# Kernel optimization log

Measured on AMD Instinct MI355X. Metric: run time of the kernel, lower is better.

Reference implementation:

```python
import jax, jax.numpy as jnp
import numpy as np

T, D = 1024, 2048
H, KH, HD = 16, 4, 128
E, K, I = 8, 2, 2048
EPS = 1e-5
CAP = 30.0          # attn logit softcap and router logit softcap
BASE = 10000.0      # rope theta


def setup_inputs() -> dict:
    key = jax.random.key(0)
    ks = jax.random.split(key, 8)
    s = 0.02
    return {
        "positions": jnp.arange(T, dtype=jnp.int32),
        "hidden_states": jax.random.normal(ks[0], (T, D), jnp.float32),
        "w_qkv": jax.random.normal(ks[1], (D, (H + 2 * KH) * HD), jnp.float32) * s,
        "w_o": jax.random.normal(ks[2], (H * HD, D), jnp.float32) * s,
        "w_gate": jax.random.normal(ks[3], (D, E), jnp.float32) * s,
        "w_gate_up": jax.random.normal(ks[4], (E, D, 2 * I), jnp.float32) * s,
        "w_down": jax.random.normal(ks[5], (E, I, D), jnp.float32) * s,
        "w_pre_attn": 1.0 + 0.01 * jax.random.normal(ks[6], (D,), jnp.float32),
        "w_post_attn": jnp.ones((D,), jnp.float32),
        "w_pre_moe": 1.0 + 0.01 * jax.random.normal(ks[7], (D,), jnp.float32),
        "w_post_moe": jnp.ones((D,), jnp.float32),
    }


def rmsnorm(x, w):
    v = jnp.mean(jnp.square(x), axis=-1, keepdims=True)
    return x * jax.lax.rsqrt(v + EPS) * w


def rope_neox(pos, x):
    # x: [T, nH, HD]; full-head-dim neox-style rotation
    half = HD // 2
    inv = 1.0 / (BASE ** (jnp.arange(half, dtype=jnp.float32) * 2.0 / HD))
    f = pos.astype(jnp.float32)[:, None] * inv            # [T, half]
    cos, sin = jnp.cos(f)[:, None, :], jnp.sin(f)[:, None, :]
    x1, x2 = x[..., :half], x[..., half:]
    return jnp.concatenate([x1 * cos - x2 * sin, x2 * cos + x1 * sin], axis=-1)


def attention(pos, x, w_qkv, w_o):
    qkv = x @ w_qkv
    q, k, v = jnp.split(qkv, [H * HD, (H + KH) * HD], axis=-1)
    q = rope_neox(pos, q.reshape(T, H, HD))
    k = rope_neox(pos, k.reshape(T, KH, HD))
    v = v.reshape(T, KH, HD)
    rep = H // KH                                          # GQA repeat
    k = jnp.repeat(k, rep, axis=1)
    v = jnp.repeat(v, rep, axis=1)
    s = jnp.einsum('qhd,khd->hqk', q, k) * (HD ** -0.5)
    s = CAP * jnp.tanh(s / CAP)                            # tanh logit cap
    causal = pos[:, None] >= pos[None, :]
    s = jnp.where(causal[None], s, -1e30)
    p = jax.nn.softmax(s, axis=-1)
    o = jnp.einsum('hqk,khd->qhd', p, v).reshape(T, H * HD)
    return o @ w_o


def moe(x, w_gate, w_gate_up, w_down):
    logits = x @ w_gate
    logits = CAP * jnp.tanh(logits / CAP)                  # router softcap
    probs = jax.nn.softmax(logits, axis=-1)
    topv, topi = jax.lax.top_k(probs, K)                   # no renorm (Grok1)
    comb = jnp.zeros((T, E), probs.dtype).at[jnp.arange(T)[:, None], topi].set(topv)
    gu = jnp.einsum('td,edf->etf', x, w_gate_up)           # [E,T,2I]
    g, u = jnp.split(gu, 2, axis=-1)
    act = jax.nn.gelu(g, approximate=True) * u             # GeluAndMul(tanh)
    out_e = jnp.einsum('eti,eid->etd', act, w_down)        # [E,T,D]
    return jnp.einsum('etd,te->td', out_e, comb)


def reference(positions, hidden_states, w_qkv, w_o, w_gate, w_gate_up, w_down,
              w_pre_attn, w_post_attn, w_pre_moe, w_post_moe):
    resid = hidden_states
    h = rmsnorm(hidden_states, w_pre_attn)
    a = attention(positions, h, w_qkv, w_o)
    resid = resid + rmsnorm(a, w_post_attn)                # post_attn_norm + add
    h = rmsnorm(resid, w_pre_moe)
    m = moe(h, w_gate, w_gate_up, w_down)
    return resid + rmsnorm(m, w_post_moe)
```

## Files before the change

### kernel.cpp

```cpp
#include <hip/hip_runtime.h>

#define TT 1024
#define DD 2048
#define NH 16
#define NKV 4
#define HDIM 128
#define NE 8
#define NI 2048
#define EPSF 1e-5f
#define NP 4

typedef short bf16x8 __attribute__((ext_vector_type(8)));
typedef float f32x4 __attribute__((ext_vector_type(4)));

__device__ __forceinline__ unsigned short f2bf(float x) {
  unsigned u = __float_as_uint(x);
  u += 0x7FFFu + ((u >> 16) & 1u);
  return (unsigned short)(u >> 16);
}
__device__ __forceinline__ float bf2f(unsigned short h) {
  return __uint_as_float((unsigned)h << 16);
}
__device__ __forceinline__ void split2(float a, unsigned short& h,
                                       unsigned short& l) {
  h = f2bf(a);
  l = f2bf(a - bf2f(h));
}

__device__ __forceinline__ float wave_sum(float v) {
#pragma unroll
  for (int m = 32; m >= 1; m >>= 1) v += __shfl_xor(v, m, 64);
  return v;
}
__device__ __forceinline__ float wave_max(float v) {
#pragma unroll
  for (int m = 32; m >= 1; m >>= 1) v = fmaxf(v, __shfl_xor(v, m, 64));
  return v;
}

__device__ __forceinline__ int swz4(int r) { return (r ^ (r >> 2)) & 3; }
__device__ __forceinline__ int swz8(int r) { return (r ^ (r >> 3)) & 7; }

__device__ __forceinline__ void stage32(char* dst, const unsigned short* src,
                                        int rs, int tid) {
#pragma unroll
  for (int j = 0; j < 2; ++j) {
    int idx = tid + j * 256;
    int r = idx >> 2, c = idx & 3;
    bf16x8 v = *(const bf16x8*)(src + r * rs + c * 8);
    *(bf16x8*)(dst + r * 64 + ((c ^ swz4(r)) << 4)) = v;
  }
}
__device__ __forceinline__ void ld_frag(const char* base, int wrow, int l15,
                                        int lg, bf16x8* dst) {
#pragma unroll
  for (int i = 0; i < 4; ++i) {
    int row = wrow + i * 16 + l15;
    dst[i] = *(const bf16x8*)(base + row * 64 + ((lg ^ swz4(row)) << 4));
  }
}
__device__ __forceinline__ void mm16(const bf16x8* xa, const bf16x8* xb,
                                     f32x4 (*acc)[4]) {
#pragma unroll
  for (int mi = 0; mi < 4; ++mi)
#pragma unroll
    for (int ni = 0; ni < 4; ++ni)
      acc[mi][ni] = __builtin_amdgcn_mfma_f32_16x16x32_bf16(
          xa[mi], xb[ni], acc[mi][ni], 0, 0, 0);
}

template <int MODE>
__global__ __launch_bounds__(256) void pgemm3_k(
    const unsigned short* __restrict__ Ah, const unsigned short* __restrict__ Al,
    const unsigned short* __restrict__ Bh, const unsigned short* __restrict__ Bl,
    float* __restrict__ C, int Kh, int lda, int ldb, int ldc, long czs,
    float escale) {
  int z = blockIdx.z;
  int m0 = blockIdx.y * 128, n0 = blockIdx.x * 128;
  int k0 = 0, kend = Kh;
  if (MODE == 0) {
    k0 = z * Kh;
    kend = k0 + Kh;
    C += (long)z * czs;
  } else if (MODE == 1) {
    if (blockIdx.x > blockIdx.y) return;
    Ah += (long)z * TT * lda;
    Al += (long)z * TT * lda;
    Bh += (long)(z >> 2) * TT * ldb;
    Bl += (long)(z >> 2) * TT * ldb;
    C += (long)z * czs;
  } else {
    int head = z >> 2, ch = z & 3;
    int limit = (blockIdx.y + 1) * 128;
    k0 = ch * 256;
    if (k0 >= limit) return;
    kend = k0 + 256 < limit ? k0 + 256 : limit;
    Ah += (long)head * TT * lda;
    Al += (long)head * TT * lda;
    Bh += (long)(head >> 2) * HDIM * ldb;
    Bl += (long)(head >> 2) * HDIM * ldb;
    C += (long)ch * czs + head * HDIM;
  }

  __shared__ __align__(16) char lds[32768];
  int tid = threadIdx.x, lane = tid & 63, wid = tid >> 6;
  int wm = (wid >> 1) * 64, wn = (wid & 1) * 64;
  int l15 = lane & 15, lg = lane >> 4;

  f32x4 acc[4][4];
#pragma unroll
  for (int i = 0; i < 4; ++i)
#pragma unroll
    for (int j = 0; j < 4; ++j) acc[i][j] = {0.f, 0.f, 0.f, 0.f};

  for (int kt = k0; kt < kend; kt += 32) {
    __syncthreads();
    stage32(lds, Ah + (long)m0 * lda + kt, lda, tid);
    stage32(lds + 8192, Al + (long)m0 * lda + kt, lda, tid);
    stage32(lds + 16384, Bh + (long)n0 * ldb + kt, ldb, tid);
    stage32(lds + 24576, Bl + (long)n0 * ldb + kt, ldb, tid);
    __syncthreads();
    bf16x8 fah[4], fal[4], fbh[4], fbl[4];
    ld_frag(lds, wm, l15, lg, fah);
    ld_frag(lds + 16384, wn, l15, lg, fbh);
    mm16(fah, fbh, acc);
    ld_frag(lds + 24576, wn, l15, lg, fbl);
    mm16(fah, fbl, acc);
    ld_frag(lds + 8192, wm, l15, lg, fal);
    mm16(fal, fbh, acc);
  }
#pragma unroll
  for (int mi = 0; mi < 4; ++mi)
#pragma unroll
    for (int ni = 0; ni < 4; ++ni)
#pragma unroll
      for (int rr = 0; rr < 4; ++rr) {
        int ml = m0 + wm + mi * 16 + lg * 4 + rr;
        int col = n0 + wn + ni * 16 + l15;
        float val = acc[mi][ni][rr];
        if (MODE == 1) {
          val *= escale;
          val = 30.f * tanhf(val * (1.f / 30.f));
        }
        C[(long)ml * ldc + col] = val;
      }
}

template <int AMODE, int EP>
__global__ __launch_bounds__(256) void gemm_k(
    const unsigned short* __restrict__ A, const float* __restrict__ Bf,
    float* __restrict__ Cf, int N, int K, int lda, int ldb, int ldc, long bzs,
    long pzs, const int* __restrict__ cnt, const int* __restrict__ basep,
    const int* __restrict__ tok, const int* __restrict__ slotp,
    const float* __restrict__ wtp, float* __restrict__ slots_out) {
  int z = blockIdx.z;
  int e = z >> 1, kp = z & 1;
  Bf += (long)e * bzs;
  int Me = cnt[e], be = basep[e];
  int m0 = blockIdx.y * 128, n0 = blockIdx.x * 128;
  if (m0 >= Me) return;
  int Kc = K >> 1, kbeg = kp * Kc, klim = kbeg + Kc;

  __shared__ __align__(16) char lds[32768];
  const int BOFF = 16384;
  int tid = threadIdx.x, lane = tid & 63, wid = tid >> 6;
  int wm = (wid >> 1) * 64, wn = (wid & 1) * 64;
  int l15 = lane & 15, lg = lane >> 4;

  f32x4 acc[4][4];
#pragma unroll
  for (int i = 0; i < 4; ++i)
#pragma unroll
    for (int j = 0; j < 4; ++j) acc[i][j] = {0.f, 0.f, 0.f, 0.f};

  for (int kt = kbeg; kt < klim; kt += 64) {
    __syncthreads();
#pragma unroll
    for (int i = 0; i < 4; ++i) {
      int idx = tid + i * 256;
      int r = idx >> 3, c = idx & 7;
      int gm = m0 + r;
      bf16x8 v = {0, 0, 0, 0, 0, 0, 0, 0};
      bool ok = gm < Me;
      long arow;
      if (AMODE == 1)
        arow = ok ? (long)tok[e * TT + gm] : 0;
      else
        arow = (long)be + gm;
      if (ok) v = *(const bf16x8*)(A + arow * (long)lda + kt + c * 8);
      *(bf16x8*)(lds + r * 128 + ((c ^ swz8(r)) << 4)) = v;
    }
#pragma unroll
    for (int i = 0; i < 4; ++i) {
      int gidx = tid + i * 256;
      int n = gidx & 127, kc = gidx >> 7;
      const float* src = Bf + (long)(kt + kc * 8) * ldb + n0 + n;
      bf16x8 v;
#pragma unroll
      for (int u = 0; u < 8; ++u)
        ((unsigned short*)&v)[u] = f2bf(src[(long)u * ldb]);
      *(bf16x8*)(lds + BOFF + n * 128 + ((kc ^ swz8(n)) << 4)) = v;
    }
    __syncthreads();
#pragma unroll
    for (int s = 0; s < 2; ++s) {
      bf16x8 af[4], bfr[4];
      int slotk = s * 4 + lg;
#pragma unroll
      for (int mi = 0; mi < 4; ++mi) {
        int row = wm + mi * 16 + l15;
        af[mi] =
            *(const bf16x8*)(lds + row * 128 + ((slotk ^ swz8(row)) << 4));
      }
#pragma unroll
      for (int ni = 0; ni < 4; ++ni) {
        int row = wn + ni * 16 + l15;
        bfr[ni] = *(const bf16x8*)(lds + BOFF + row * 128 +
                                   ((slotk ^ swz8(row)) << 4));
      }
      mm16(af, bfr, acc);
    }
  }
#pragma unroll
  for (int mi = 0; mi < 4; ++mi)
#pragma unroll
    for (int ni = 0; ni < 4; ++ni)
#pragma unroll
      for (int rr = 0; rr < 4; ++rr) {
        int ml = m0 + wm + mi * 16 + lg * 4 + rr;
        int col = n0 + wn + ni * 16 + l15;
        float val = acc[mi][ni][rr];
        if (ml < Me) {
          if (EP == 0) {
            Cf[(long)kp * pzs + (long)(be + ml) * ldc + col] = val;
          } else {
            int t = tok[e * TT + ml];
            int s = slotp[e * TT + ml];
            float w = wtp[e * TT + ml];
            slots_out[(long)kp * pzs + ((long)s * TT + t) * DD + col] =
                val * w;
          }
        }
      }
}

__global__ __launch_bounds__(256) void tsplit_k(const float* __restrict__ W,
                                                unsigned short* __restrict__ Th,
                                                unsigned short* __restrict__ Tl,
                                                int K, int N) {
  __shared__ float lds[64 * 65];
  int n0 = blockIdx.x * 64, k0 = blockIdx.y * 64;
  int tid = threadIdx.x;
#pragma unroll
  for (int i = 0; i < 4; ++i) {
    int idx = tid + i * 256;
    int kr = idx >> 4, cg = idx & 15;
    float4 v = *(const float4*)(W + (long)(k0 + kr) * N + n0 + cg * 4);
    float* p = &lds[kr * 65 + cg * 4];
    p[0] = v.x; p[1] = v.y; p[2] = v.z; p[3] = v.w;
  }
  __syncthreads();
#pragma unroll
  for (int i = 0; i < 2; ++i) {
    int idx = tid + i * 256;
    int n = idx >> 3, kc = idx & 7;
    bf16x8 h8, l8;
#pragma unroll
    for (int u = 0; u < 8; ++u) {
      unsigned short hh, ll;
      split2(lds[(kc * 8 + u) * 65 + n], hh, ll);
      ((unsigned short*)&h8)[u] = hh;
      ((unsigned short*)&l8)[u] = ll;
    }
    long o = (long)(n0 + n) * K + k0 + kc * 8;
    *(bf16x8*)(Th + o) = h8;
    *(bf16x8*)(Tl + o) = l8;
  }
}

__global__ __launch_bounds__(256) void rms_pre_k(const float* __restrict__ x,
                                                 const float* __restrict__ w,
                                                 unsigned short* __restrict__ oh,
                                                 unsigned short* __restrict__ ol) {
  __shared__ float red[4];
  int t = blockIdx.x, tid = threadIdx.x;
  const float* xr = x + (long)t * DD;
  float xv[8];
  float ss = 0.f;
#pragma unroll
  for (int i = 0; i < 8; ++i) {
    float v = xr[tid + i * 256];
    xv[i] = v;
    ss += v * v;
  }
  ss = wave_sum(ss);
  if ((tid & 63) == 0) red[tid >> 6] = ss;
  __syncthreads();
  float r = rsqrtf((red[0] + red[1] + red[2] + red[3]) * (1.f / DD) + EPSF);
#pragma unroll
  for (int i = 0; i < 8; ++i) {
    int d = tid + i * 256;
    split2(xv[i] * r * w[d], oh[(long)t * DD + d], ol[(long)t * DD + d]);
  }
}

__global__ __launch_bounds__(256) void rope_qk_k(
    const int* __restrict__ pos, const float* __restrict__ qp,
    unsigned short* __restrict__ qh, unsigned short* __restrict__ ql,
    unsigned short* __restrict__ kh, unsigned short* __restrict__ kl) {
  __shared__ float cs[64], sn[64];
  int t = blockIdx.x, tid = threadIdx.x;
  float pf = (float)pos[t];
  if (tid < 64) {
    float inv = exp2f(-(float)tid * 0.20762050593046015f);
    float f = pf * inv;
    cs[tid] = cosf(f);
    sn[tid] = sinf(f);
  }
  __syncthreads();
  const float* row = qp + (long)t * 3072;
  const long PS = (long)TT * 3072;
#pragma unroll
  for (int i = 0; i < 4; ++i) {
    int idx = tid + i * 256;
    int h = idx >> 6, j = idx & 63;
    float x1 = 0.f, x2 = 0.f;
#pragma unroll
    for (int p = 0; p < NP; ++p) {
      x1 += row[p * PS + h * HDIM + j];
      x2 += row[p * PS + h * HDIM + 64 + j];
    }
    float c = cs[j], s = sn[j];
    long base = ((long)h * TT + t) * HDIM;
    split2(x1 * c - x2 * s, qh[base + j], ql[base + j]);
    split2(x2 * c + x1 * s, qh[base + 64 + j], ql[base + 64 + j]);
  }
  {
    int k2 = tid >> 6, j = tid & 63;
    float x1 = 0.f, x2 = 0.f;
#pragma unroll
    for (int p = 0; p < NP; ++p) {
      x1 += row[p * PS + 2048 + k2 * HDIM + j];
      x2 += row[p * PS + 2048 + k2 * HDIM + 64 + j];
    }
    float c = cs[j], s = sn[j];
    long base = ((long)k2 * TT + t) * HDIM;
    split2(x1 * c - x2 * s, kh[base + j], kl[base + j]);
    split2(x2 * c + x1 * s, kh[base + 64 + j], kl[base + 64 + j]);
  }
}

__global__ __launch_bounds__(256) void vtrans_k(const float* __restrict__ qp,
                                                unsigned short* __restrict__ Vh,
                                                unsigned short* __restrict__ Vl) {
  __shared__ float lds[64 * 129];
  int tb = blockIdx.x, kv = blockIdx.y;
  int t0 = tb * 128;
  int tid = threadIdx.x;
  const long PS = (long)TT * 3072;
#pragma unroll
  for (int dh = 0; dh < 2; ++dh) {
    if (dh) __syncthreads();
#pragma unroll
    for (int i = 0; i < 8; ++i) {
      int fidx = tid + i * 256;
      int t = fidx >> 4, dq = fidx & 15;
      long gi = (long)(t0 + t) * 3072 + 2560 + kv * HDIM + dh * 64 + dq * 4;
      float4 a = *(const float4*)(qp + gi);
#pragma unroll
      for (int p = 1; p < NP; ++p) {
        float4 b = *(const float4*)(qp + p * PS + gi);
        a.x += b.x; a.y += b.y; a.z += b.z; a.w += b.w;
      }
      lds[(dq * 4 + 0) * 129 + t] = a.x;
      lds[(dq * 4 + 1) * 129 + t] = a.y;
      lds[(dq * 4 + 2) * 129 + t] = a.z;
      lds[(dq * 4 + 3) * 129 + t] = a.w;
    }
    __syncthreads();
#pragma unroll
    for (int i = 0; i < 4; ++i) {
      int cidx = tid + i * 256;
      int d = cidx >> 4, tc = cidx & 15;
      bf16x8 h8, l8;
#pragma unroll
      for (int u = 0; u < 8; ++u) {
        unsigned short hh, ll;
        split2(lds[d * 129 + tc * 8 + u], hh, ll);
        ((unsigned short*)&h8)[u] = hh;
        ((unsigned short*)&l8)[u] = ll;
      }
      long o = ((long)kv * HDIM + dh * 64 + d) * TT + t0 + tc * 8;
      *(bf16x8*)(Vh + o) = h8;
      *(bf16x8*)(Vl + o) = l8;
    }
  }
}

__global__ __launch_bounds__(256) void softmax_k(const float* __restrict__ S,
                                                 unsigned short* __restrict__ Ph,
                                                 unsigned short* __restrict__ Pl) {
  __shared__ float red[4];
  int i = blockIdx.x, h = blockIdx.y, tid = threadIdx.x;
  int len = i + 1;
  int wlimit = ((i >> 7) + 1) << 7;
  const float* srow = S + ((long)h * TT + i) * TT;
  unsigned short* ph = Ph + ((long)h * TT + i) * TT;
  unsigned short* pl = Pl + ((long)h * TT + i) * TT;
  float m = -1e30f;
  for (int j = tid; j < len; j += 256) m = fmaxf(m, srow[j]);
  m = wave_max(m);
  if ((tid & 63) == 0) red[tid >> 6] = m;
  __syncthreads();
  m = fmaxf(fmaxf(red[0], red[1]), fmaxf(red[2], red[3]));
  __syncthreads();
  float ssum = 0.f;
  for (int j = tid; j < len; j += 256) ssum += expf(srow[j] - m);
  ssum = wave_sum(ssum);
  if ((tid & 63) == 0) red[tid >> 6] = ssum;
  __syncthreads();
  float inv = 1.f / (red[0] + red[1] + red[2] + red[3]);
  for (int j = tid; j < wlimit; j += 256) {
    float p = (j < len) ? expf(srow[j] - m) * inv : 0.f;
    unsigned short hh, ll;
    split2(p, hh, ll);
    ph[j] = hh;
    pl[j] = ll;
  }
}

__global__ __launch_bounds__(256) void obreduce_k(const float* __restrict__ obp,
                                                  unsigned short* __restrict__ oh,
                                                  unsigned short* __restrict__ ol) {
  int m = blockIdx.x, tid = threadIdx.x;
  int nv = ((m >> 7) >> 1) + 1;
#pragma unroll
  for (int i = 0; i < 8; ++i) {
    int d = tid + i * 256;
    float s = 0.f;
    for (int c = 0; c < nv; ++c) s += obp[(long)c * TT * DD + (long)m * DD + d];
    split2(s, oh[(long)m * DD + d], ol[(long)m * DD + d]);
  }
}

__global__ __launch_bounds__(256) void post_attn_k(
    const float* __restrict__ ap, const float* __restrict__ hidden,
    const float* __restrict__ w_post, const float* __restrict__ w_pre2,
    float* __restrict__ resid1, float* __restrict__ h2f,
    unsigned short* __restrict__ h2b) {
  __shared__ float red[4];
  int t = blockIdx.x, tid = threadIdx.x;
  const long PS = (long)TT * DD;
  float av[8];
  float ss = 0.f;
#pragma unroll
  for (int i = 0; i < 8; ++i) {
    long o = (long)t * DD + tid + i * 256;
    float v = 0.f;
#pragma unroll
    for (int p = 0; p < NP; ++p) v += ap[p * PS + o];
    av[i] = v;
    ss += v * v;
  }
  ss = wave_sum(ss);
  if ((tid & 63) == 0) red[tid >> 6] = ss;
  __syncthreads();
  float r1 = rsqrtf((red[0] + red[1] + red[2] + red[3]) * (1.f / DD) + EPSF);
  __syncthreads();
  float rv[8];
  float ss2 = 0.f;
#pragma unroll
  for (int i = 0; i < 8; ++i) {
    int d = tid + i * 256;
    float v = hidden[(long)t * DD + d] + av[i] * r1 * w_post[d];
    rv[i] = v;
    resid1[(long)t * DD + d] = v;
    ss2 += v * v;
  }
  ss2 = wave_sum(ss2);
  if ((tid & 63) == 0) red[tid >> 6] = ss2;
  __syncthreads();
  float r2 = rsqrtf((red[0] + red[1] + red[2] + red[3]) * (1.f / DD) + EPSF);
#pragma unroll
  for (int i = 0; i < 8; ++i) {
    int d = tid + i * 256;
    float hv = rv[i] * r2 * w_pre2[d];
    h2f[(long)t * DD + d] = hv;
    h2b[(long)t * DD + d] = f2bf(hv);
  }
}

__global__ __launch_bounds__(256) void gate_k(const float* __restrict__ h2f,
                                              const float* __restrict__ wg,
                                              int* cnt, int* tok, int* slotp,
                                              float* wtp) {
  __shared__ float red[4][8];
  int t = blockIdx.x, tid = threadIdx.x;
  float a[8] = {0, 0, 0, 0, 0, 0, 0, 0};
  const float* x = h2f + (long)t * DD;
  for (int d = tid; d < DD; d += 256) {
    float xv = x[d];
    const float* wr = wg + d * 8;
#pragma unroll
    for (int e = 0; e < 8; ++e) a[e] += xv * wr[e];
  }
#pragma unroll
  for (int e = 0; e < 8; ++e) a[e] = wave_sum(a[e]);
  if ((tid & 63) == 0) {
#pragma unroll
    for (int e = 0; e < 8; ++e) red[tid >> 6][e] = a[e];
  }
  __syncthreads();
  if (tid == 0) {
    float l[8], p[8];
    float m = -1e30f;
    for (int e = 0; e < 8; ++e) {
      float v = red[0][e] + red[1][e] + red[2][e] + red[3][e];
      v = 30.f * tanhf(v * (1.f / 30.f));
      l[e] = v;
      m = fmaxf(m, v);
    }
    float s = 0.f;
    for (int e = 0; e < 8; ++e) { p[e] = expf(l[e] - m); s += p[e]; }
    for (int e = 0; e < 8; ++e) p[e] /= s;
    int i1 = 0;
    for (int e = 1; e < 8; ++e) if (p[e] > p[i1]) i1 = e;
    int i2 = (i1 == 0) ? 1 : 0;
    for (int e = 0; e < 8; ++e) if (e != i1 && p[e] > p[i2]) i2 = e;
    int q1 = atomicAdd(&cnt[i1], 1);
    tok[i1 * TT + q1] = t; slotp[i1 * TT + q1] = 0; wtp[i1 * TT + q1] = p[i1];
    int q2 = atomicAdd(&cnt[i2], 1);
    tok[i2 * TT + q2] = t; slotp[i2 * TT + q2] = 1; wtp[i2 * TT + q2] = p[i2];
  }
}

__global__ void scan_k(const int* __restrict__ cnt, int* __restrict__ basep) {
  if (threadIdx.x == 0) {
    int s = 0;
    for (int e = 0; e < NE; ++e) { basep[e] = s; s += cnt[e]; }
    basep[NE] = s;
  }
}

__global__ __launch_bounds__(256) void act_k(const float* __restrict__ gu,
                                             unsigned short* __restrict__ actb) {
  long a = blockIdx.x;
  const long PS = (long)2 * TT * 2 * NI;
  const float* g0 = gu + a * (2 * NI);
  const float* g1 = g0 + PS;
  for (int i = threadIdx.x; i < NI; i += 256) {
    float gg = g0[i] + g1[i];
    float uu = g0[i + NI] + g1[i + NI];
    float c = gg + 0.044715f * gg * gg * gg;
    float act = 0.5f * gg * (1.f + tanhf(0.7978845608028654f * c));
    actb[a * NI + i] = f2bf(act * uu);
  }
}

__global__ __launch_bounds__(256) void final_k(const float* __restrict__ resid1,
                                               const float* __restrict__ slots,
                                               const float* __restrict__ w2,
                                               float* __restrict__ out) {
  __shared__ float red[4];
  int t = blockIdx.x, tid = threadIdx.x;
  const long PL = (long)TT * DD;
  float mv[8];
  float ss = 0.f;
#pragma unroll
  for (int i = 0; i < 8; ++i) {
    long o = (long)t * DD + tid + i * 256;
    float v = slots[o] + slots[PL + o] + slots[2 * PL + o] + slots[3 * PL + o];
    mv[i] = v;
    ss += v * v;
  }
  ss = wave_sum(ss);
  if ((tid & 63) == 0) red[tid >> 6] = ss;
  __syncthreads();
  float r = rsqrtf((red[0] + red[1] + red[2] + red[3]) * (1.f / DD) + EPSF);
#pragma unroll
  for (int i = 0; i < 8; ++i) {
    int d = tid + i * 256;
    out[(long)t * DD + d] = resid1[(long)t * DD + d] + mv[i] * r * w2[d];
  }
}

__global__ void sentinel_k(float* out) { out[threadIdx.x] = 12345.0f; }

extern "C" void kernel_launch(void* const* d_in, const int* in_sizes, int n_in,
                              void* d_out, int out_size, void* d_ws,
                              size_t ws_size, hipStream_t stream) {
  const int* pos = (const int*)d_in[0];
  const float* hidden = (const float*)d_in[1];
  const float* w_qkv = (const float*)d_in[2];
  const float* w_o = (const float*)d_in[3];
  const float* w_gate = (const float*)d_in[4];
  const float* w_gu = (const float*)d_in[5];
  const float* w_down = (const float*)d_in[6];
  const float* w_pre_attn = (const float*)d_in[7];
  const float* w_post_attn = (const float*)d_in[8];
  const float* w_pre_moe = (const float*)d_in[9];
  const float* w_post_moe = (const float*)d_in[10];
  float* out = (float*)d_out;

  char* ws = (char*)d_ws;
  size_t off = 0;
  auto alloc = [&](size_t bytes) {
    char* p = ws + off;
    off += (bytes + 255) & ~(size_t)255;
    return p;
  };
  typedef unsigned short u16;
  u16* h1h = (u16*)alloc((size_t)TT * DD * 2);
  u16* h1l = (u16*)alloc((size_t)TT * DD * 2);
  u16* wqkvTh = (u16*)alloc((size_t)3072 * DD * 2);
  u16* wqkvTl = (u16*)alloc((size_t)3072 * DD * 2);
  float* qkvp = (float*)alloc((size_t)NP * TT * 3072 * 4);
  u16* qh_ = (u16*)alloc((size_t)NH * TT * HDIM * 2);
  u16* ql_ = (u16*)alloc((size_t)NH * TT * HDIM * 2);
  u16* kh_ = (u16*)alloc((size_t)NKV * TT * HDIM * 2);
  u16* kl_ = (u16*)alloc((size_t)NKV * TT * HDIM * 2);
  u16* vth = (u16*)alloc((size_t)NKV * HDIM * TT * 2);
  u16* vtl = (u16*)alloc((size_t)NKV * HDIM * TT * 2);
  float* S = (float*)alloc((size_t)NH * TT * TT * 4);
  u16* Ph = (u16*)alloc((size_t)NH * TT * TT * 2);
  u16* Pl = (u16*)alloc((size_t)NH * TT * TT * 2);
  float* obp = (float*)alloc((size_t)4 * TT * DD * 4);
  u16* obh = (u16*)alloc((size_t)TT * DD * 2);
  u16* obl = (u16*)alloc((size_t)TT * DD * 2);
  u16* woTh = (u16*)alloc((size_t)DD * DD * 2);
  u16* woTl = (u16*)alloc((size_t)DD * DD * 2);
  float* attnp = (float*)alloc((size_t)NP * TT * DD * 4);
  float* resid1 = (float*)alloc((size_t)TT * DD * 4);
  float* h2f = (float*)alloc((size_t)TT * DD * 4);
  u16* h2b = (u16*)alloc((size_t)TT * DD * 2);
  int* cnt = (int*)alloc(NE * 4);
  int* basep = (int*)alloc((NE + 1) * 4);
  int* tok = (int*)alloc((size_t)NE * TT * 4);
  int* slotp = (int*)alloc((size_t)NE * TT * 4);
  float* wtp = (float*)alloc((size_t)NE * TT * 4);
  float* gu = (float*)alloc((size_t)2 * 2 * TT * 2 * NI * 4);
  u16* actb = (u16*)alloc((size_t)2 * TT * NI * 2);
  float* slots = (float*)alloc((size_t)2 * 2 * TT * DD * 4);

  if (off > ws_size) {
    sentinel_k<<<1, 256, 0, stream>>>(out);
    return;
  }

  hipMemsetAsync(cnt, 0, NE * 4, stream);
  dim3 blk(256);

  rms_pre_k<<<TT, blk, 0, stream>>>(hidden, w_pre_attn, h1h, h1l);
  tsplit_k<<<dim3(3072 / 64, DD / 64), blk, 0, stream>>>(w_qkv, wqkvTh, wqkvTl,
                                                         DD, 3072);
  tsplit_k<<<dim3(DD / 64, DD / 64), blk, 0, stream>>>(w_o, woTh, woTl, DD, DD);

  pgemm3_k<0><<<dim3(3072 / 128, TT / 128, NP), blk, 0, stream>>>(
      h1h, h1l, wqkvTh, wqkvTl, qkvp, DD / NP, DD, DD, 3072, (long)TT * 3072,
      0.f);

  rope_qk_k<<<TT, blk, 0, stream>>>(pos, qkvp, qh_, ql_, kh_, kl_);
  vtrans_k<<<dim3(8, NKV), blk, 0, stream>>>(qkvp, vth, vtl);

  pgemm3_k<1><<<dim3(TT / 128, TT / 128, NH), blk, 0, stream>>>(
      qh_, ql_, kh_, kl_, S, HDIM, HDIM, HDIM, TT, (long)TT * TT,
      0.08838834764831845f);

  softmax_k<<<dim3(TT, NH), blk, 0, stream>>>(S, Ph, Pl);

  pgemm3_k<2><<<dim3(1, TT / 128, NH * 4), blk, 0, stream>>>(
      Ph, Pl, vth, vtl, obp, 256, TT, TT, DD, (long)TT * DD, 0.f);
  obreduce_k<<<TT, blk, 0, stream>>>(obp, obh, obl);

  pgemm3_k<0><<<dim3(DD / 128, TT / 128, NP), blk, 0, stream>>>(
      obh, obl, woTh, woTl, attnp, DD / NP, DD, DD, DD, (long)TT * DD, 0.f);

  post_attn_k<<<TT, blk, 0, stream>>>(attnp, hidden, w_post_attn, w_pre_moe,
                                      resid1, h2f, h2b);
  gate_k<<<TT, blk, 0, stream>>>(h2f, w_gate, cnt, tok, slotp, wtp);
  scan_k<<<1, 64, 0, stream>>>(cnt, basep);

  gemm_k<1, 0><<<dim3(2 * NI / 128, TT / 128, NE * 2), blk, 0, stream>>>(
      h2b, w_gu, gu, 2 * NI, DD, DD, 2 * NI, 2 * NI, (long)DD * 2 * NI,
      (long)2 * TT * 2 * NI, cnt, basep, tok, nullptr, nullptr, nullptr);

  act_k<<<2 * TT, blk, 0, stream>>>(gu, actb);

  gemm_k<2, 3><<<dim3(DD / 128, TT / 128, NE * 2), blk, 0, stream>>>(
      actb, w_down, nullptr, DD, NI, NI, DD, DD, (long)NI * DD,
      (long)2 * TT * DD, cnt, basep, tok, slotp, wtp, slots);

  final_k<<<TT, blk, 0, stream>>>(resid1, slots, w_post_moe, out);
}
```

Measured before the change: 491.2 us.

## Process two M-blocks per MoE GEMM block and store intermediates as bf16

The MoE expert GEMM now handles up to 256 token rows per block in two 128-row sub-tiles. Each fp32-to-bf16 converted weight tile is loaded once and reused across both sub-tiles, which halves the redundant weight reads and conversions. The gate/up partials and down-projection slot outputs are also written as bf16 instead of fp32, reducing intermediate memory traffic for act_k and final_k. The cost is doubled accumulator registers and more LDS, which may lower occupancy, plus some extra rounding in the partial sums.

```diff
diff --git a/kernel.cpp b/kernel.cpp
--- a/kernel.cpp
+++ b/kernel.cpp
@@ -149,47 +149,36 @@
 template <int AMODE, int EP>
 __global__ __launch_bounds__(256) void gemm_k(
     const unsigned short* __restrict__ A, const float* __restrict__ Bf,
-    float* __restrict__ Cf, int N, int K, int lda, int ldb, int ldc, long bzs,
-    long pzs, const int* __restrict__ cnt, const int* __restrict__ basep,
-    const int* __restrict__ tok, const int* __restrict__ slotp,
-    const float* __restrict__ wtp, float* __restrict__ slots_out) {
+    unsigned short* __restrict__ Cb, int N, int K, int lda, int ldb, int ldc,
+    long bzs, long pzs, const int* __restrict__ cnt,
+    const int* __restrict__ basep, const int* __restrict__ tok,
+    const int* __restrict__ slotp, const float* __restrict__ wtp,
+    unsigned short* __restrict__ slots_out) {
   int z = blockIdx.z;
   int e = z >> 1, kp = z & 1;
   Bf += (long)e * bzs;
   int Me = cnt[e], be = basep[e];
-  int m0 = blockIdx.y * 128, n0 = blockIdx.x * 128;
-  if (m0 >= Me) return;
+  int ms0 = blockIdx.y * 256, n0 = blockIdx.x * 128;
+  if (ms0 >= Me) return;
+  int nmb = (Me - ms0 > 128) ? 2 : 1;
   int Kc = K >> 1, kbeg = kp * Kc, klim = kbeg + Kc;
 
-  __shared__ __align__(16) char lds[32768];
-  const int BOFF = 16384;
+  __shared__ __align__(16) char lds[49152];
+  const int BOFF = 32768;
   int tid = threadIdx.x, lane = tid & 63, wid = tid >> 6;
   int wm = (wid >> 1) * 64, wn = (wid & 1) * 64;
   int l15 = lane & 15, lg = lane >> 4;
 
-  f32x4 acc[4][4];
-#pragma unroll
-  for (int i = 0; i < 4; ++i)
-#pragma unroll
-    for (int j = 0; j < 4; ++j) acc[i][j] = {0.f, 0.f, 0.f, 0.f};
+  f32x4 acc[2][4][4];
+#pragma unroll
+  for (int b = 0; b < 2; ++b)
+#pragma unroll
+    for (int i = 0; i < 4; ++i)
+#pragma unroll
+      for (int j = 0; j < 4; ++j) acc[b][i][j] = {0.f, 0.f, 0.f, 0.f};
 
   for (int kt = kbeg; kt < klim; kt += 64) {
     __syncthreads();
-#pragma unroll
-    for (int i = 0; i < 4; ++i) {
-      int idx = tid + i * 256;
-      int r = idx >> 3, c = idx & 7;
-      int gm = m0 + r;
-      bf16x8 v = {0, 0, 0, 0, 0, 0, 0, 0};
-      bool ok = gm < Me;
-      long arow;
-      if (AMODE == 1)
-        arow = ok ? (long)tok[e * TT + gm] : 0;
-      else
-        arow = (long)be + gm;
-      if (ok) v = *(const bf16x8*)(A + arow * (long)lda + kt + c * 8);
-      *(bf16x8*)(lds + r * 128 + ((c ^ swz8(r)) << 4)) = v;
-    }
 #pragma unroll
     for (int i = 0; i < 4; ++i) {
       int gidx = tid + i * 256;
@@ -201,47 +190,75 @@
         ((unsigned short*)&v)[u] = f2bf(src[(long)u * ldb]);
       *(bf16x8*)(lds + BOFF + n * 128 + ((kc ^ swz8(n)) << 4)) = v;
     }
+    for (int mb = 0; mb < nmb; ++mb) {
+#pragma unroll
+      for (int i = 0; i < 4; ++i) {
+        int idx = tid + i * 256;
+        int r = idx >> 3, c = idx & 7;
+        int gm = ms0 + mb * 128 + r;
+        bf16x8 v = {0, 0, 0, 0, 0, 0, 0, 0};
+        bool ok = gm < Me;
+        long arow;
+        if (AMODE == 1)
+          arow = ok ? (long)tok[e * TT + gm] : 0;
+        else
+          arow = (long)be + gm;
+        if (ok) v = *(const bf16x8*)(A + arow * (long)lda + kt + c * 8);
+        *(bf16x8*)(lds + mb * 16384 + r * 128 + ((c ^ swz8(r)) << 4)) = v;
+      }
+    }
     __syncthreads();
 #pragma unroll
     for (int s = 0; s < 2; ++s) {
-      bf16x8 af[4], bfr[4];
       int slotk = s * 4 + lg;
-#pragma unroll
-      for (int mi = 0; mi < 4; ++mi) {
-        int row = wm + mi * 16 + l15;
-        af[mi] =
-            *(const bf16x8*)(lds + row * 128 + ((slotk ^ swz8(row)) << 4));
-      }
+      bf16x8 bfr[4];
 #pragma unroll
       for (int ni = 0; ni < 4; ++ni) {
         int row = wn + ni * 16 + l15;
         bfr[ni] = *(const bf16x8*)(lds + BOFF + row * 128 +
                                    ((slotk ^ swz8(row)) << 4));
       }
-      mm16(af, bfr, acc);
-    }
-  }
-#pragma unroll
-  for (int mi = 0; mi < 4; ++mi)
-#pragma unroll
-    for (int ni = 0; ni < 4; ++ni)
-#pragma unroll
-      for (int rr = 0; rr < 4; ++rr) {
-        int ml = m0 + wm + mi * 16 + lg * 4 + rr;
-        int col = n0 + wn + ni * 16 + l15;
-        float val = acc[mi][ni][rr];
-        if (ml < Me) {
-          if (EP == 0) {
-            Cf[(long)kp * pzs + (long)(be + ml) * ldc + col] = val;
-          } else {
-            int t = tok[e * TT + ml];
-            int s = slotp[e * TT + ml];
-            float w = wtp[e * TT + ml];
-            slots_out[(long)kp * pzs + ((long)s * TT + t) * DD + col] =
-                val * w;
+#pragma unroll
+      for (int mb = 0; mb < 2; ++mb) {
+        if (mb < nmb) {
+          bf16x8 af[4];
+#pragma unroll
+          for (int mi = 0; mi < 4; ++mi) {
+            int row = wm + mi * 16 + l15;
+            af[mi] = *(const bf16x8*)(lds + mb * 16384 + row * 128 +
+                                      ((slotk ^ swz8(row)) << 4));
           }
+          mm16(af, bfr, acc[mb]);
         }
       }
+    }
+  }
+#pragma unroll
+  for (int mb = 0; mb < 2; ++mb) {
+    if (mb < nmb) {
+#pragma unroll
+      for (int mi = 0; mi < 4; ++mi)
+#pragma unroll
+        for (int ni = 0; ni < 4; ++ni)
+#pragma unroll
+          for (int rr = 0; rr < 4; ++rr) {
+            int ml = ms0 + mb * 128 + wm + mi * 16 + lg * 4 + rr;
+            int col = n0 + wn + ni * 16 + l15;
+            float val = acc[mb][mi][ni][rr];
+            if (ml < Me) {
+              if (EP == 0) {
+                Cb[(long)kp * pzs + (long)(be + ml) * ldc + col] = f2bf(val);
+              } else {
+                int t = tok[e * TT + ml];
+                int s = slotp[e * TT + ml];
+                float w = wtp[e * TT + ml];
+                slots_out[(long)kp * pzs + ((long)s * TT + t) * DD + col] =
+                    f2bf(val * w);
+              }
+            }
+          }
+    }
+  }
 }
 
 __global__ __launch_bounds__(256) void tsplit_k(const float* __restrict__ W,
@@ -542,25 +559,24 @@
   }
 }
 
-__global__ __launch_bounds__(256) void act_k(const float* __restrict__ gu,
+__global__ __launch_bounds__(256) void act_k(const unsigned short* __restrict__ gu,
                                              unsigned short* __restrict__ actb) {
   long a = blockIdx.x;
   const long PS = (long)2 * TT * 2 * NI;
-  const float* g0 = gu + a * (2 * NI);
-  const float* g1 = g0 + PS;
+  const unsigned short* g0 = gu + a * (2 * NI);
+  const unsigned short* g1 = g0 + PS;
   for (int i = threadIdx.x; i < NI; i += 256) {
-    float gg = g0[i] + g1[i];
-    float uu = g0[i + NI] + g1[i + NI];
+    float gg = bf2f(g0[i]) + bf2f(g1[i]);
+    float uu = bf2f(g0[i + NI]) + bf2f(g1[i + NI]);
     float c = gg + 0.044715f * gg * gg * gg;
     float act = 0.5f * gg * (1.f + tanhf(0.7978845608028654f * c));
     actb[a * NI + i] = f2bf(act * uu);
   }
 }
 
-__global__ __launch_bounds__(256) void final_k(const float* __restrict__ resid1,
-                                               const float* __restrict__ slots,
-                                               const float* __restrict__ w2,
-                                               float* __restrict__ out) {
+__global__ __launch_bounds__(256) void final_k(
+    const float* __restrict__ resid1, const unsigned short* __restrict__ slots,
+    const float* __restrict__ w2, float* __restrict__ out) {
   __shared__ float red[4];
   int t = blockIdx.x, tid = threadIdx.x;
   const long PL = (long)TT * DD;
@@ -569,7 +585,8 @@
 #pragma unroll
   for (int i = 0; i < 8; ++i) {
     long o = (long)t * DD + tid + i * 256;
-    float v = slots[o] + slots[PL + o] + slots[2 * PL + o] + slots[3 * PL + o];
+    float v = bf2f(slots[o]) + bf2f(slots[PL + o]) + bf2f(slots[2 * PL + o]) +
+              bf2f(slots[3 * PL + o]);
     mv[i] = v;
     ss += v * v;
   }
@@ -638,9 +655,9 @@
   int* tok = (int*)alloc((size_t)NE * TT * 4);
   int* slotp = (int*)alloc((size_t)NE * TT * 4);
   float* wtp = (float*)alloc((size_t)NE * TT * 4);
-  float* gu = (float*)alloc((size_t)2 * 2 * TT * 2 * NI * 4);
+  u16* gu = (u16*)alloc((size_t)2 * 2 * TT * 2 * NI * 2);
   u16* actb = (u16*)alloc((size_t)2 * TT * NI * 2);
-  float* slots = (float*)alloc((size_t)2 * 2 * TT * DD * 4);
+  u16* slots = (u16*)alloc((size_t)2 * 2 * TT * DD * 2);
 
   if (off > ws_size) {
     sentinel_k<<<1, 256, 0, stream>>>(out);
@@ -680,13 +697,13 @@
   gate_k<<<TT, blk, 0, stream>>>(h2f, w_gate, cnt, tok, slotp, wtp);
   scan_k<<<1, 64, 0, stream>>>(cnt, basep);
 
-  gemm_k<1, 0><<<dim3(2 * NI / 128, TT / 128, NE * 2), blk, 0, stream>>>(
+  gemm_k<1, 0><<<dim3(2 * NI / 128, TT / 256, NE * 2), blk, 0, stream>>>(
       h2b, w_gu, gu, 2 * NI, DD, DD, 2 * NI, 2 * NI, (long)DD * 2 * NI,
       (long)2 * TT * 2 * NI, cnt, basep, tok, nullptr, nullptr, nullptr);
 
   act_k<<<2 * TT, blk, 0, stream>>>(gu, actb);
 
-  gemm_k<2, 3><<<dim3(DD / 128, TT / 128, NE * 2), blk, 0, stream>>>(
+  gemm_k<2, 3><<<dim3(DD / 128, TT / 256, NE * 2), blk, 0, stream>>>(
       actb, w_down, nullptr, DD, NI, NI, DD, DD, (long)NI * DD,
       (long)2 * TT * DD, cnt, basep, tok, slotp, wtp, slots);
 
```

New measurement: 740.3 us. +50.7%, slower.
